# Optimization experiments

Hardware: AMD Instinct MI355X
Metric: run time of the kernel (lower is better)

Reference implementation:

```python
import jax, jax.numpy as jnp
import numpy as np

B, N, DIM = 8, 4096, 768
HEADS = 12
HEAD_DIM = DIM // HEADS  # 64
EXP = 2                  # expansion_ratio
EDIM = EXP * DIM         # 1536


def setup_inputs() -> dict:
    key = jax.random.key(0)
    ks = jax.random.split(key, 7)
    s = lambda fan_in: 1.0 / np.sqrt(fan_in)
    return {
        "x": jax.random.normal(ks[0], (B, N, DIM), jnp.float32),
        "w_q": jax.random.normal(ks[1], (DIM, DIM), jnp.float32) * s(DIM),
        "w_kv": jax.random.normal(ks[2], (DIM, 2 * DIM), jnp.float32) * s(DIM),
        "w_proj": jax.random.normal(ks[3], (EDIM, DIM), jnp.float32) * s(EDIM),
        "b_proj": jax.random.normal(ks[4], (DIM,), jnp.float32) * 0.01,
        "w_lepe": jax.random.normal(ks[5], (EDIM, 1, 3, 3), jnp.float32) * s(9),
        "b_lepe": jax.random.normal(ks[6], (EDIM,), jnp.float32) * 0.01,
    }


def _expand_heads(t):
    # t: (B, M, C). roll last axis by -head_dim//2 (the i=1 step of the
    # head-expansion trick with r_int=2), concat -> (B, M, 2C), then split
    # into 2*HEADS heads of HEAD_DIM and move heads to axis 1.
    rolled = jnp.roll(t, -(HEAD_DIM // 2), axis=-1)
    e = jnp.concatenate([t, rolled], axis=-1)  # (B, M, 2C)
    Bb, M, _ = e.shape
    return jnp.swapaxes(e.reshape(Bb, M, EXP * HEADS, HEAD_DIM), 1, 2)  # (B, 2h, M, d)


def reference(x, w_q, w_kv, w_proj, b_proj, w_lepe, b_lepe):
    Bb, Nn, C = x.shape
    ed = EXP * C
    # kv projection -> k, v: (B, h, N, d)
    kv = (x @ w_kv).reshape(Bb, Nn, 2, HEADS, HEAD_DIM)
    k = jnp.swapaxes(kv[:, :, 0], 1, 2)
    v = jnp.swapaxes(kv[:, :, 1], 1, 2)
    # q projection + head expansion -> (B, 2h, N, d)
    q = x @ w_q
    eq = _expand_heads(q)
    # LePE: depthwise 3x3 conv on expanded_q laid out as (B, 2C, H, W)
    H = int(round(Nn ** 0.5))
    qc = jnp.swapaxes(eq, 2, 3).reshape(Bb, ed, H, H)
    lepe = jax.lax.conv_general_dilated(
        qc, w_lepe, window_strides=(1, 1), padding='SAME',
        dimension_numbers=('NCHW', 'OIHW', 'NCHW'), feature_group_count=ed)
    lepe = (lepe + b_lepe[None, :, None, None]).reshape(Bb, ed, Nn)
    lepe = jnp.swapaxes(lepe, 1, 2)  # (B, N, 2C)
    # linear attention: softmax over head_dim, precompute K^T V (d x d)
    ks = jax.nn.softmax(k, axis=3)                      # softmax over feature dim d
    ktv = jnp.einsum('bhnd,bhne->bhde', ks, v)          # (B, h, d, d)
    ektv = _expand_heads(jnp.swapaxes(ktv, 1, 2).reshape(Bb, HEAD_DIM, C))  # (B, 2h, d, d)
    attn = jnp.einsum('bhnd,bhde->bhne', eq, ektv)      # (B, 2h, N, d)
    scale = HEAD_DIM ** -0.5
    out = jnp.swapaxes(scale * attn, 1, 2).reshape(Bb, Nn, ed)  # (B, N, 2C)
    return (out + lepe) @ w_proj + b_proj
```

## Files before the change

### kernel.cpp

```cpp
#include <hip/hip_runtime.h>

#define NB 8
#define NTOK 4096
#define CDIM 768
#define EDIM 1536
#define NHEADS 12
#define HD 64
#define TOTTOK (NB * NTOK)

typedef float floatx4 __attribute__((ext_vector_type(4)));
typedef __bf16 bf16x8 __attribute__((ext_vector_type(8)));

__device__ __forceinline__ void gld16(const __bf16* g, void* l) {
  __builtin_amdgcn_global_load_lds(
      (const __attribute__((address_space(1))) unsigned int*)g,
      (__attribute__((address_space(3))) unsigned int*)l, 16, 0, 0);
}

#define MFMA16(a, b, c) __builtin_amdgcn_mfma_f32_16x16x32_bf16(a, b, c, 0, 0, 0)
#define FENCE() asm volatile("" ::: "memory")
#define BARRIER() do { FENCE(); __builtin_amdgcn_s_barrier(); FENCE(); } while (0)

__global__ __launch_bounds__(256) void f32_to_bf16_kernel(
    const float* __restrict__ in, __bf16* __restrict__ out, long n) {
  long i = ((long)blockIdx.x * 256 + threadIdx.x) * 4;
  if (i >= n) return;
  float4 f = *(const float4*)(in + i);
  alignas(8) __bf16 h[4];
  h[0] = (__bf16)f.x; h[1] = (__bf16)f.y; h[2] = (__bf16)f.z; h[3] = (__bf16)f.w;
  *(unsigned long long*)(out + i) = *(const unsigned long long*)h;
}

__global__ __launch_bounds__(256) void transpose_w_kernel(
    const float* __restrict__ W, __bf16* __restrict__ Wt, int K, int N) {
  __shared__ float tile[32][33];
  int nb = blockIdx.x * 32, kb = blockIdx.y * 32;
  int tx = threadIdx.x & 31, ty = threadIdx.x >> 5;
  #pragma unroll
  for (int i = ty; i < 32; i += 8)
    tile[i][tx] = W[(long)(kb + i) * N + nb + tx];
  __syncthreads();
  #pragma unroll
  for (int i = ty; i < 32; i += 8)
    Wt[(long)(nb + i) * K + kb + tx] = (__bf16)tile[tx][i];
}

__global__ __launch_bounds__(512, 2) void gemm256_kernel(
    const __bf16* __restrict__ A, const __bf16* __restrict__ Bt,
    void* __restrict__ C0, void* __restrict__ C1,
    const float* __restrict__ bias,
    int M, int N, int K, int nxb, int mode) {
  __shared__ __bf16 As[2][256 * 64];
  __shared__ __bf16 Bs[2][256 * 64];
  const int tid = threadIdx.x;
  const int wave = tid >> 6, lane = tid & 63;

  const int flat = blockIdx.x;
  const int xcd = flat & 7, rem = flat >> 3;
  const int per = (M >> 8) >> 3;
  const int yb = xcd * per + rem / nxb;
  const int xb = rem % nxb;
  const long m0 = (long)yb * 256;
  const int n0 = xb * 256;

  const int wm = (wave >> 2) * 128;
  const int wn = (wave & 3) * 64;

  const int srow = lane >> 3;
  const int gchunk = (lane & 7) ^ srow;
  const __bf16* Ag = A + (m0 + wave * 8 + srow) * (long)K + gchunk * 8;
  const __bf16* Bg = Bt + ((long)n0 + wave * 8 + srow) * (long)K + gchunk * 8;
  const long slabK = 64 * (long)K;

  const int fr = lane & 15, qh = lane >> 4;
  const int c0 = ((qh ^ (fr & 7)) << 3);
  const int c1 = (((qh + 4) ^ (fr & 7)) << 3);

  floatx4 acc[8][4] = {};
  bf16x8 afl[4][2], bf01[2][2], bf23[2][2];
  const int nt = K >> 6;

  {
    char* al = (char*)&As[0][0] + wave * 1024;
    char* bl = (char*)&Bs[0][0] + wave * 1024;
    gld16(Bg + 0 * slabK, bl + 0 * 8192);
    gld16(Bg + 1 * slabK, bl + 1 * 8192);
    gld16(Bg + 2 * slabK, bl + 2 * 8192);
    gld16(Bg + 3 * slabK, bl + 3 * 8192);
    gld16(Ag + 0 * slabK, al + 0 * 8192);
    gld16(Ag + 2 * slabK, al + 2 * 8192);
    gld16(Ag + 1 * slabK, al + 1 * 8192);
    gld16(Ag + 3 * slabK, al + 3 * 8192);
  }
  asm volatile("s_waitcnt vmcnt(2)" ::: "memory");
  BARRIER();

  for (int t = 0; t < nt; ++t) {
    const int cur = t & 1;
    const bool pf = (t + 1 < nt);
    const __bf16* Ac = &As[cur][0];
    const __bf16* Bc = &Bs[cur][0];
    const __bf16* an = Ag + (t + 1) * 64;
    const __bf16* bn = Bg + (t + 1) * 64;
    char* al = (char*)&As[cur ^ 1][0] + wave * 1024;
    char* bl = (char*)&Bs[cur ^ 1][0] + wave * 1024;

    #pragma unroll
    for (int i = 0; i < 4; ++i) {
      const __bf16* p = &Ac[(wm + i * 16 + fr) * 64];
      afl[i][0] = *(const bf16x8*)(p + c0);
      afl[i][1] = *(const bf16x8*)(p + c1);
    }
    #pragma unroll
    for (int j = 0; j < 2; ++j) {
      const __bf16* p = &Bc[(wn + j * 16 + fr) * 64];
      bf01[j][0] = *(const bf16x8*)(p + c0);
      bf01[j][1] = *(const bf16x8*)(p + c1);
    }
    if (pf) { gld16(bn + 0 * slabK, bl + 0 * 8192);
              gld16(bn + 1 * slabK, bl + 1 * 8192); }
    BARRIER();
    asm volatile("s_waitcnt lgkmcnt(0)");
    __builtin_amdgcn_sched_barrier(0);
    __builtin_amdgcn_s_setprio(1);
    #pragma unroll
    for (int i = 0; i < 4; ++i)
      #pragma unroll
      for (int j = 0; j < 2; ++j) {
        acc[i][j] = MFMA16(afl[i][0], bf01[j][0], acc[i][j]);
        acc[i][j] = MFMA16(afl[i][1], bf01[j][1], acc[i][j]);
      }
    __builtin_amdgcn_s_setprio(0);
    BARRIER();

    #pragma unroll
    for (int j = 0; j < 2; ++j) {
      const __bf16* p = &Bc[(wn + (2 + j) * 16 + fr) * 64];
      bf23[j][0] = *(const bf16x8*)(p + c0);
      bf23[j][1] = *(const bf16x8*)(p + c1);
    }
    if (pf) {
      gld16(bn + 2 * slabK, bl + 2 * 8192);
      gld16(bn + 3 * slabK, bl + 3 * 8192);
      asm volatile("s_waitcnt vmcnt(4)" ::: "memory");
    } else {
      asm volatile("s_waitcnt vmcnt(0)" ::: "memory");
    }
    BARRIER();
    asm volatile("s_waitcnt lgkmcnt(0)");
    __builtin_amdgcn_sched_barrier(0);
    __builtin_amdgcn_s_setprio(1);
    #pragma unroll
    for (int i = 0; i < 4; ++i)
      #pragma unroll
      for (int j = 0; j < 2; ++j) {
        acc[i][2 + j] = MFMA16(afl[i][0], bf23[j][0], acc[i][2 + j]);
        acc[i][2 + j] = MFMA16(afl[i][1], bf23[j][1], acc[i][2 + j]);
      }
    __builtin_amdgcn_s_setprio(0);
    BARRIER();

    #pragma unroll
    for (int i = 0; i < 4; ++i) {
      const __bf16* p = &Ac[(wm + (4 + i) * 16 + fr) * 64];
      afl[i][0] = *(const bf16x8*)(p + c0);
      afl[i][1] = *(const bf16x8*)(p + c1);
    }
    if (pf) { gld16(an + 0 * slabK, al + 0 * 8192);
              gld16(an + 2 * slabK, al + 2 * 8192); }
    BARRIER();
    asm volatile("s_waitcnt lgkmcnt(0)");
    __builtin_amdgcn_sched_barrier(0);
    __builtin_amdgcn_s_setprio(1);
    #pragma unroll
    for (int i = 0; i < 4; ++i)
      #pragma unroll
      for (int j = 0; j < 2; ++j) {
        acc[4 + i][2 + j] = MFMA16(afl[i][0], bf23[j][0], acc[4 + i][2 + j]);
        acc[4 + i][2 + j] = MFMA16(afl[i][1], bf23[j][1], acc[4 + i][2 + j]);
      }
    __builtin_amdgcn_s_setprio(0);
    BARRIER();

    if (pf) {
      gld16(an + 1 * slabK, al + 1 * 8192);
      gld16(an + 3 * slabK, al + 3 * 8192);
      asm volatile("s_waitcnt vmcnt(2)" ::: "memory");
    }
    BARRIER();
    asm volatile("s_waitcnt lgkmcnt(0)");
    __builtin_amdgcn_sched_barrier(0);
    __builtin_amdgcn_s_setprio(1);
    #pragma unroll
    for (int i = 0; i < 4; ++i)
      #pragma unroll
      for (int j = 0; j < 2; ++j) {
        acc[4 + i][j] = MFMA16(afl[i][0], bf01[j][0], acc[4 + i][j]);
        acc[4 + i][j] = MFMA16(afl[i][1], bf01[j][1], acc[4 + i][j]);
      }
    __builtin_amdgcn_s_setprio(0);
    BARRIER();
  }

  const int col = lane & 15, rq = (lane >> 4) * 4;
  if (mode == 1) {
    #pragma unroll
    for (int j = 0; j < 4; ++j) {
      const int gn = n0 + wn + j * 16 + col;
      const float bj = bias[gn];
      #pragma unroll
      for (int i = 0; i < 8; ++i)
        #pragma unroll
        for (int r = 0; r < 4; ++r)
          ((float*)C0)[(m0 + wm + i * 16 + rq + r) * (long)N + gn] =
              acc[i][j][r] + bj;
    }
  } else if (n0 + 256 <= CDIM) {
    #pragma unroll
    for (int j = 0; j < 4; ++j) {
      const int gn = n0 + wn + j * 16 + col;
      #pragma unroll
      for (int i = 0; i < 8; ++i)
        #pragma unroll
        for (int r = 0; r < 4; ++r)
          ((__bf16*)C0)[(m0 + wm + i * 16 + rq + r) * (long)CDIM + gn] =
              (__bf16)acc[i][j][r];
    }
  } else {
    #pragma unroll
    for (int j = 0; j < 4; ++j) {
      const int gn = n0 + wn + j * 16 + col - CDIM;
      #pragma unroll
      for (int i = 0; i < 8; ++i)
        #pragma unroll
        for (int r = 0; r < 4; ++r)
          ((__bf16*)C1)[(m0 + wm + i * 16 + rq + r) * (long)EDIM + gn] =
              (__bf16)acc[i][j][r];
    }
  }
}

__global__ __launch_bounds__(256) void gemm_glds_kernel(
    const __bf16* __restrict__ A, const __bf16* __restrict__ Bt,
    void* __restrict__ C0, void* __restrict__ C1,
    const float* __restrict__ bias,
    int M, int N, int K, int nxb, int mode) {
  __shared__ __bf16 As[128 * 32];
  __shared__ __bf16 Bs[128 * 32];
  const int tid = threadIdx.x;
  const int wave = tid >> 6, lane = tid & 63;

  const int flat = blockIdx.x;
  const int xcd = flat & 7, rem = flat >> 3;
  const int per = (M >> 7) >> 3;
  const int yb = xcd * per + rem / nxb;
  const int xb = rem % nxb;
  const long m0 = (long)yb * 128;
  const int n0 = xb * 128;

  const int wm = (wave >> 1) * 64, wn = (wave & 1) * 64;

  const int srow = lane >> 2;
  const int gchunk = (lane & 3) ^ ((lane >> 3) & 3);
  const __bf16* Ag = A + (m0 + wave * 16 + srow) * (long)K + gchunk * 8;
  const __bf16* Bg = Bt + ((long)n0 + wave * 16 + srow) * (long)K + gchunk * 8;
  char* Al = (char*)As + wave * 16 * 64;
  char* Bl = (char*)Bs + wave * 16 * 64;
  const long rowskip = 64 * (long)K;

  const int fr = lane & 15;
  const int csw = ((lane >> 4) ^ ((fr >> 1) & 3)) * 8;

  floatx4 acc[4][4] = {};

  for (int k0 = 0; k0 < K; k0 += 32) {
    __syncthreads();
    gld16(Ag + k0, Al);
    gld16(Ag + k0 + rowskip, Al + 64 * 64);
    gld16(Bg + k0, Bl);
    gld16(Bg + k0 + rowskip, Bl + 64 * 64);
    __syncthreads();
    bf16x8 af[4], bfr[4];
    #pragma unroll
    for (int i = 0; i < 4; ++i)
      af[i] = *(const bf16x8*)&As[(wm + i * 16 + fr) * 32 + csw];
    #pragma unroll
    for (int j = 0; j < 4; ++j)
      bfr[j] = *(const bf16x8*)&Bs[(wn + j * 16 + fr) * 32 + csw];
    #pragma unroll
    for (int i = 0; i < 4; ++i)
      #pragma unroll
      for (int j = 0; j < 4; ++j)
        acc[i][j] = __builtin_amdgcn_mfma_f32_16x16x32_bf16(af[i], bfr[j], acc[i][j], 0, 0, 0);
  }

  const int col = lane & 15, rq = (lane >> 4) * 4;
  if (mode == 1) {
    #pragma unroll
    for (int i = 0; i < 4; ++i)
      #pragma unroll
      for (int j = 0; j < 4; ++j)
        #pragma unroll
        for (int r = 0; r < 4; ++r) {
          long gm = m0 + wm + i * 16 + rq + r;
          int gn = n0 + wn + j * 16 + col;
          ((float*)C0)[gm * N + gn] = acc[i][j][r] + bias[gn];
        }
  } else {
    if (n0 + 128 <= CDIM) {
      #pragma unroll
      for (int i = 0; i < 4; ++i)
        #pragma unroll
        for (int j = 0; j < 4; ++j)
          #pragma unroll
          for (int r = 0; r < 4; ++r) {
            long gm = m0 + wm + i * 16 + rq + r;
            int gn = n0 + wn + j * 16 + col;
            ((__bf16*)C0)[gm * CDIM + gn] = (__bf16)acc[i][j][r];
          }
    } else {
      #pragma unroll
      for (int i = 0; i < 4; ++i)
        #pragma unroll
        for (int j = 0; j < 4; ++j)
          #pragma unroll
          for (int r = 0; r < 4; ++r) {
            long gm = m0 + wm + i * 16 + rq + r;
            int gn = n0 + wn + j * 16 + col - CDIM;
            ((__bf16*)C1)[gm * EDIM + gn] = (__bf16)acc[i][j][r];
          }
    }
  }
}

__global__ __launch_bounds__(256) void ktv_kernel(
    const __bf16* __restrict__ kv, float* __restrict__ ktv_part) {
  const int split = blockIdx.x, h = blockIdx.y, b = blockIdx.z;
  __shared__ __bf16 As[64 * 40];
  __shared__ __bf16 Bs[64 * 40];
  const int tid = threadIdx.x, wave = tid >> 6, lane = tid & 63;
  const int sn = tid >> 3;
  const int sc = (tid & 7) * 8;
  const int fr = lane & 15, fk = (lane >> 4) * 8;
  floatx4 acc[4] = {};
  const long rowbase = (long)b * NTOK * EDIM;

  for (int n0 = split * 1024; n0 < split * 1024 + 1024; n0 += 32) {
    __syncthreads();
    const __bf16* krow = kv + rowbase + (long)(n0 + sn) * EDIM + h * HD + sc;
    const __bf16* vrow = krow + CDIM;
    uint4 ku = *(const uint4*)krow;
    uint4 vu = *(const uint4*)vrow;
    const __bf16* kh = (const __bf16*)&ku;
    const __bf16* vh = (const __bf16*)&vu;
    float kf[8];
    float mx = -1e30f;
    #pragma unroll
    for (int j = 0; j < 8; ++j) { kf[j] = (float)kh[j]; mx = fmaxf(mx, kf[j]); }
    #pragma unroll
    for (int m = 1; m < 8; m <<= 1) mx = fmaxf(mx, __shfl_xor(mx, m));
    float s = 0.f;
    #pragma unroll
    for (int j = 0; j < 8; ++j) { kf[j] = __expf(kf[j] - mx); s += kf[j]; }
    #pragma unroll
    for (int m = 1; m < 8; m <<= 1) s += __shfl_xor(s, m);
    const float inv = 1.f / s;
    #pragma unroll
    for (int j = 0; j < 8; ++j) {
      As[(sc + j) * 40 + sn] = (__bf16)(kf[j] * inv);
      Bs[(sc + j) * 40 + sn] = vh[j];
    }
    __syncthreads();
    bf16x8 af = *(const bf16x8*)&As[(wave * 16 + fr) * 40 + fk];
    #pragma unroll
    for (int j = 0; j < 4; ++j) {
      bf16x8 bf_ = *(const bf16x8*)&Bs[(j * 16 + fr) * 40 + fk];
      acc[j] = __builtin_amdgcn_mfma_f32_16x16x32_bf16(af, bf_, acc[j], 0, 0, 0);
    }
  }

  const int col = lane & 15, rq = (lane >> 4) * 4;
  long base = (((long)split * NB + b) * NHEADS + h) * (HD * HD);
  #pragma unroll
  for (int j = 0; j < 4; ++j)
    #pragma unroll
    for (int r = 0; r < 4; ++r)
      ktv_part[base + (wave * 16 + rq + r) * HD + j * 16 + col] = acc[j][r];
}

__global__ __launch_bounds__(256) void ektv_kernel(
    const float* __restrict__ ktv_part, __bf16* __restrict__ ektv) {
  int idx = blockIdx.x * 256 + threadIdx.x;
  int e = idx & 63;
  int d = (idx >> 6) & 63;
  int H = (idx >> 12) % 24;
  int b = idx / 98304;
  int c = H * 64 + e;
  int cp = (c < CDIM) ? c : (c - CDIM + 32) % CDIM;
  int hs = cp >> 6, es = cp & 63;
  long o = (((long)b * NHEADS + hs) * HD + d) * HD + es;
  float s = 0.f;
  #pragma unroll
  for (int sp = 0; sp < 4; ++sp)
    s += ktv_part[(long)sp * (NB * NHEADS * HD * HD) + o];
  long ob = ((long)(idx >> 12)) * (HD * HD) + (long)e * HD + d;
  ektv[ob] = (__bf16)s;
}

__global__ __launch_bounds__(256) void attn_kernel(
    const __bf16* __restrict__ q, const __bf16* __restrict__ ektv,
    __bf16* __restrict__ mid) {
  const int tt = blockIdx.x, H = blockIdx.y, b = blockIdx.z;
  __shared__ __bf16 As[128 * 72];
  __shared__ __bf16 Bs[64 * 72];
  const int tid = threadIdx.x, wave = tid >> 6, lane = tid & 63;
  const int qbase = (H < NHEADS) ? H * 64 : (H - NHEADS) * 64 + 32;
  const long n0 = (long)b * NTOK + tt * 128;

  {
    int nl = tid >> 1, d0 = (tid & 1) * 32;
    const __bf16* qrow = q + (n0 + nl) * CDIM;
    #pragma unroll
    for (int cch = 0; cch < 4; ++cch) {
      int d = d0 + cch * 8;
      int c0 = qbase + d;
      if (c0 >= CDIM) c0 -= CDIM;
      *(uint4*)&As[nl * 72 + d] = *(const uint4*)(qrow + c0);
    }
  }
  {
    int e = tid >> 2, ch4 = (tid & 3) * 8;
    const __bf16* src = ektv + ((long)b * 24 + H) * (HD * HD) + e * HD;
    *(uint4*)&Bs[e * 72 + ch4] = *(const uint4*)(src + ch4);
    *(uint4*)&Bs[e * 72 + ch4 + 32] = *(const uint4*)(src + ch4 + 32);
  }
  __syncthreads();

  floatx4 acc[2][4] = {};
  const int fr = lane & 15, fk = (lane >> 4) * 8;
  const int wm = wave * 32;
  #pragma unroll
  for (int kk = 0; kk < 64; kk += 32) {
    bf16x8 af0 = *(const bf16x8*)&As[(wm + fr) * 72 + kk + fk];
    bf16x8 af1 = *(const bf16x8*)&As[(wm + 16 + fr) * 72 + kk + fk];
    #pragma unroll
    for (int j = 0; j < 4; ++j) {
      bf16x8 bf_ = *(const bf16x8*)&Bs[(j * 16 + fr) * 72 + kk + fk];
      acc[0][j] = __builtin_amdgcn_mfma_f32_16x16x32_bf16(af0, bf_, acc[0][j], 0, 0, 0);
      acc[1][j] = __builtin_amdgcn_mfma_f32_16x16x32_bf16(af1, bf_, acc[1][j], 0, 0, 0);
    }
  }

  const int col = lane & 15, rq = (lane >> 4) * 4;
  const float scale = 0.125f;
  #pragma unroll
  for (int i = 0; i < 2; ++i)
    #pragma unroll
    for (int j = 0; j < 4; ++j)
      #pragma unroll
      for (int r = 0; r < 4; ++r) {
        long n = n0 + wm + i * 16 + rq + r;
        mid[n * EDIM + H * 64 + j * 16 + col] = (__bf16)(acc[i][j][r] * scale);
      }
}

__global__ __launch_bounds__(256) void lepe_kernel(
    const __bf16* __restrict__ q, const float* __restrict__ w_lepe,
    const float* __restrict__ b_lepe, __bf16* __restrict__ mid) {
  __shared__ __bf16 smem[6 * 64 * 64];
  const int g = blockIdx.x, yg = blockIdx.y, b = blockIdx.z;
  const int y0 = yg * 4;
  const int tid = threadIdx.x;

  #pragma unroll
  for (int k = 0; k < 12; ++k) {
    int v = tid + k * 256;
    int r = v >> 9;
    int rem = v & 511;
    int x = rem >> 3;
    int chv = (rem & 7) * 8;
    int yy = y0 + r - 1;
    uint4 val = {0u, 0u, 0u, 0u};
    if (yy >= 0 && yy < 64)
      val = *(const uint4*)(q + ((long)(b * NTOK + yy * 64 + x)) * CDIM + g * 64 + chv);
    *(uint4*)&smem[r * 4096 + x * 64 + chv] = val;
  }
  __syncthreads();

  const int ch = tid & 63, xg = tid >> 6;
  const int cq = g * 64 + ch;
  const int c2 = CDIM + ((cq + 736) % CDIM);
  float w1[9], w2[9];
  #pragma unroll
  for (int j = 0; j < 9; ++j) {
    w1[j] = w_lepe[cq * 9 + j];
    w2[j] = w_lepe[c2 * 9 + j];
  }
  const float bias1 = b_lepe[cq], bias2 = b_lepe[c2];

  const int x0 = xg * 16;
  float cm[6], cc[6], cp[6];
  #pragma unroll
  for (int r = 0; r < 6; ++r) {
    cm[r] = (x0 > 0) ? (float)smem[r * 4096 + (x0 - 1) * 64 + ch] : 0.f;
    cc[r] = (float)smem[r * 4096 + x0 * 64 + ch];
  }
  #pragma unroll
  for (int i = 0; i < 16; ++i) {
    const int x = x0 + i;
    #pragma unroll
    for (int r = 0; r < 6; ++r)
      cp[r] = (x < 63) ? (float)smem[r * 4096 + (x + 1) * 64 + ch] : 0.f;
    #pragma unroll
    for (int ly = 0; ly < 4; ++ly) {
      float a1 = bias1, a2 = bias2;
      #pragma unroll
      for (int r = 0; r < 3; ++r) {
        const float vm = cm[ly + r], vc = cc[ly + r], vp = cp[ly + r];
        a1 += w1[r * 3 + 0] * vm + w1[r * 3 + 1] * vc + w1[r * 3 + 2] * vp;
        a2 += w2[r * 3 + 0] * vm + w2[r * 3 + 1] * vc + w2[r * 3 + 2] * vp;
      }
      long o = ((long)(b * NTOK + (y0 + ly) * 64 + x)) * EDIM;
      mid[o + cq] = (__bf16)((float)mid[o + cq] + a1);
      mid[o + c2] = (__bf16)((float)mid[o + c2] + a2);
    }
    #pragma unroll
    for (int r = 0; r < 6; ++r) { cm[r] = cc[r]; cc[r] = cp[r]; }
  }
}

extern "C" void kernel_launch(void* const* d_in, const int* in_sizes, int n_in,
                              void* d_out, int out_size, void* d_ws, size_t ws_size,
                              hipStream_t stream) {
  const float* x      = (const float*)d_in[0];
  const float* w_q    = (const float*)d_in[1];
  const float* w_kv   = (const float*)d_in[2];
  const float* w_proj = (const float*)d_in[3];
  const float* b_proj = (const float*)d_in[4];
  const float* w_lepe = (const float*)d_in[5];
  const float* b_lepe = (const float*)d_in[6];
  float* out = (float*)d_out;

  char* ws = (char*)d_ws;
  __bf16* Wt_qkv = (__bf16*)ws; ws += (long)(CDIM + EDIM) * CDIM * 2;
  __bf16* Wt_p   = (__bf16*)ws; ws += (long)CDIM * EDIM * 2;
  __bf16* xb     = (__bf16*)ws; ws += (long)TOTTOK * CDIM * 2;
  __bf16* qb     = (__bf16*)ws; ws += (long)TOTTOK * CDIM * 2;
  __bf16* kvb    = (__bf16*)ws; ws += (long)TOTTOK * EDIM * 2;
  float*  ktv_part = (float*)ws; ws += (long)4 * NB * NHEADS * HD * HD * 4;
  __bf16* ektv   = (__bf16*)ws; ws += (long)NB * 24 * HD * HD * 2;
  __bf16* mid = kvb;

  f32_to_bf16_kernel<<<(TOTTOK * CDIM) / (256 * 4), 256, 0, stream>>>(
      x, xb, (long)TOTTOK * CDIM);
  transpose_w_kernel<<<dim3(CDIM / 32, CDIM / 32), 256, 0, stream>>>(
      w_q, Wt_qkv, CDIM, CDIM);
  transpose_w_kernel<<<dim3(EDIM / 32, CDIM / 32), 256, 0, stream>>>(
      w_kv, Wt_qkv + (long)CDIM * CDIM, CDIM, EDIM);
  transpose_w_kernel<<<dim3(CDIM / 32, EDIM / 32), 256, 0, stream>>>(
      w_proj, Wt_p, EDIM, CDIM);
  gemm256_kernel<<<(TOTTOK / 256) * 9, 512, 0, stream>>>(
      xb, Wt_qkv, qb, kvb, nullptr, TOTTOK, CDIM + EDIM, CDIM, 9, 0);
  ktv_kernel<<<dim3(4, NHEADS, NB), 256, 0, stream>>>(kvb, ktv_part);
  ektv_kernel<<<(NB * 24 * HD * HD) / 256, 256, 0, stream>>>(ktv_part, ektv);
  attn_kernel<<<dim3(NTOK / 128, 24, NB), 256, 0, stream>>>(qb, ektv, mid);
  lepe_kernel<<<dim3(12, 16, NB), 256, 0, stream>>>(qb, w_lepe, b_lepe, mid);
  gemm_glds_kernel<<<(TOTTOK / 128) * 6, 256, 0, stream>>>(
      mid, Wt_p, out, nullptr, b_proj, TOTTOK, CDIM, EDIM, 6, 1);
}
```

Before: 628.0 us.

## Stage GEMM bf16 epilogue through LDS for coalesced stores; split KtV reduction finer

The bf16 epilogue of the fused QKV GEMM now writes each 16-row accumulator tile into a per-wave LDS scratch area, then reads it back as 16-byte vectors so each lane stores contiguous 8-element chunks to global memory instead of scattered 2-byte stores. The K^T V kernel's token split goes from 4 to 8 partitions, doubling the grid to use more CUs, with the ektv reduction summing 8 partials. This adds LDS traffic and waitcnt stalls in the epilogue, and more partial-sum memory and reduction work.

```diff
diff --git a/kernel.cpp b/kernel.cpp
--- a/kernel.cpp
+++ b/kernel.cpp
@@ -7,6 +7,7 @@
 #define NHEADS 12
 #define HD 64
 #define TOTTOK (NB * NTOK)
+#define KSPLIT 8
 
 typedef float floatx4 __attribute__((ext_vector_type(4)));
 typedef __bf16 bf16x8 __attribute__((ext_vector_type(8)));
@@ -215,27 +216,29 @@
           ((float*)C0)[(m0 + wm + i * 16 + rq + r) * (long)N + gn] =
               acc[i][j][r] + bj;
     }
-  } else if (n0 + 256 <= CDIM) {
-    #pragma unroll
-    for (int j = 0; j < 4; ++j) {
-      const int gn = n0 + wn + j * 16 + col;
-      #pragma unroll
-      for (int i = 0; i < 8; ++i)
+  } else {
+    const bool qhalf = (n0 + 256 <= CDIM);
+    __bf16* Cb = qhalf ? (__bf16*)C0 : (__bf16*)C1;
+    const long cstride = qhalf ? CDIM : EDIM;
+    const int ncol0 = qhalf ? (n0 + wn) : (n0 + wn - CDIM);
+    __bf16* S = &As[0][0] + wave * (16 * 76);
+    const int er = lane >> 2, ec = (lane & 3) * 8;
+    #pragma unroll
+    for (int i = 0; i < 8; ++i) {
+      #pragma unroll
+      for (int j = 0; j < 4; ++j)
         #pragma unroll
         for (int r = 0; r < 4; ++r)
-          ((__bf16*)C0)[(m0 + wm + i * 16 + rq + r) * (long)CDIM + gn] =
-              (__bf16)acc[i][j][r];
-    }
-  } else {
-    #pragma unroll
-    for (int j = 0; j < 4; ++j) {
-      const int gn = n0 + wn + j * 16 + col - CDIM;
-      #pragma unroll
-      for (int i = 0; i < 8; ++i)
-        #pragma unroll
-        for (int r = 0; r < 4; ++r)
-          ((__bf16*)C1)[(m0 + wm + i * 16 + rq + r) * (long)EDIM + gn] =
-              (__bf16)acc[i][j][r];
+          S[(rq + r) * 76 + j * 16 + col] = (__bf16)acc[i][j][r];
+      asm volatile("s_waitcnt lgkmcnt(0)" ::: "memory");
+      __builtin_amdgcn_sched_barrier(0);
+      uint4 v0 = *(const uint4*)&S[er * 76 + ec];
+      uint4 v1 = *(const uint4*)&S[er * 76 + ec + 32];
+      __bf16* dst = Cb + (m0 + wm + i * 16 + er) * cstride + ncol0;
+      *(uint4*)(dst + ec) = v0;
+      *(uint4*)(dst + ec + 32) = v1;
+      asm volatile("s_waitcnt lgkmcnt(0)" ::: "memory");
+      __builtin_amdgcn_sched_barrier(0);
     }
   }
 }
@@ -344,8 +347,9 @@
   const int fr = lane & 15, fk = (lane >> 4) * 8;
   floatx4 acc[4] = {};
   const long rowbase = (long)b * NTOK * EDIM;
-
-  for (int n0 = split * 1024; n0 < split * 1024 + 1024; n0 += 32) {
+  const int span = NTOK / KSPLIT;
+
+  for (int n0 = split * span; n0 < split * span + span; n0 += 32) {
     __syncthreads();
     const __bf16* krow = kv + rowbase + (long)(n0 + sn) * EDIM + h * HD + sc;
     const __bf16* vrow = krow + CDIM;
@@ -401,7 +405,7 @@
   long o = (((long)b * NHEADS + hs) * HD + d) * HD + es;
   float s = 0.f;
   #pragma unroll
-  for (int sp = 0; sp < 4; ++sp)
+  for (int sp = 0; sp < KSPLIT; ++sp)
     s += ktv_part[(long)sp * (NB * NHEADS * HD * HD) + o];
   long ob = ((long)(idx >> 12)) * (HD * HD) + (long)e * HD + d;
   ektv[ob] = (__bf16)s;
@@ -547,7 +551,7 @@
   __bf16* xb     = (__bf16*)ws; ws += (long)TOTTOK * CDIM * 2;
   __bf16* qb     = (__bf16*)ws; ws += (long)TOTTOK * CDIM * 2;
   __bf16* kvb    = (__bf16*)ws; ws += (long)TOTTOK * EDIM * 2;
-  float*  ktv_part = (float*)ws; ws += (long)4 * NB * NHEADS * HD * HD * 4;
+  float*  ktv_part = (float*)ws; ws += (long)KSPLIT * NB * NHEADS * HD * HD * 4;
   __bf16* ektv   = (__bf16*)ws; ws += (long)NB * 24 * HD * HD * 2;
   __bf16* mid = kvb;
 
@@ -561,7 +565,7 @@
       w_proj, Wt_p, EDIM, CDIM);
   gemm256_kernel<<<(TOTTOK / 256) * 9, 512, 0, stream>>>(
       xb, Wt_qkv, qb, kvb, nullptr, TOTTOK, CDIM + EDIM, CDIM, 9, 0);
-  ktv_kernel<<<dim3(4, NHEADS, NB), 256, 0, stream>>>(kvb, ktv_part);
+  ktv_kernel<<<dim3(KSPLIT, NHEADS, NB), 256, 0, stream>>>(kvb, ktv_part);
   ektv_kernel<<<(NB * 24 * HD * HD) / 256, 256, 0, stream>>>(ktv_part, ektv);
   attn_kernel<<<dim3(NTOK / 128, 24, NB), 256, 0, stream>>>(qb, ektv, mid);
   lepe_kernel<<<dim3(12, 16, NB), 256, 0, stream>>>(qb, w_lepe, b_lepe, mid);
```

After: 595.9 us. -5.1%, faster.
